# Kernel tuning notes

Hardware: AMD Instinct MI355X
Metric: run time of the kernel (lower is better)

## Reference

```python
import math
import jax, jax.numpy as jnp
import numpy as np

B, S, D = 4, 2048, 512
H = 8
HD = D // H  # 64


def setup_inputs() -> dict:
    key = jax.random.key(0)
    k1, k2, k3, k4, k5 = jax.random.split(key, 5)
    x = jax.random.normal(k1, (B, S, D), dtype=jnp.float32)
    # additive causal mask, broadcast over [H, B, S, S] in the original code
    neg_inf = jnp.float32(-1e9)
    mask = jnp.where(jnp.tril(jnp.ones((S, S), dtype=bool)), 0.0, neg_inf).astype(jnp.float32)
    Wqkv = jax.random.normal(k2, (D, 3 * D), dtype=jnp.float32) * (1.0 / math.sqrt(D))
    bqkv = jax.random.normal(k3, (3 * D,), dtype=jnp.float32) * 0.02
    Wo = jax.random.normal(k4, (D, D), dtype=jnp.float32) * (1.0 / math.sqrt(D))
    bo = jax.random.normal(k5, (D,), dtype=jnp.float32) * 0.02
    return {"x": x, "mask": mask, "Wqkv": Wqkv, "bqkv": bqkv, "Wo": Wo, "bo": bo}


def reference(x, mask, Wqkv, bqkv, Wo, bo):
    b, s, d = x.shape
    hd = d // H
    qkv = x @ Wqkv + bqkv                       # [b, s, 3d]
    # match torch: reshape to [b, s, H, 3*hd], move heads, chunk last dim
    qkv = qkv.reshape(b, s, H, 3 * hd).transpose(0, 2, 1, 3)  # [b, H, s, 3hd]
    q, k, v = jnp.split(qkv, 3, axis=-1)        # each [b, H, s, hd]
    scale = 1.0 / math.sqrt(hd)
    scores = jnp.einsum('bhqd,bhkd->bhqk', q, k) * scale
    scores = scores + mask                      # mask [s, s] broadcasts over [b, H, s, s]
    attn = jax.nn.softmax(scores, axis=-1)
    vals = jnp.einsum('bhqk,bhkd->bhqd', attn, v)
    vals = vals.transpose(0, 2, 1, 3).reshape(b, s, d)
    return vals @ Wo + bo
```

## Files before the change

### kernel.cpp

```cpp
#include <hip/hip_runtime.h>
#include <hip/hip_bf16.h>

#define S_ 2048
#define D_ 512
#define HD_ 64
#define HH_ 8
#define M_ 8192

typedef __attribute__((ext_vector_type(8))) short short8;
typedef __attribute__((ext_vector_type(4))) short short4v;
typedef __attribute__((ext_vector_type(4))) float f32x4;

__device__ __forceinline__ unsigned short f2bf(float f) {
  unsigned u = __builtin_bit_cast(unsigned, f);
  u += 0x7fffu + ((u >> 16) & 1u);
  return (unsigned short)(u >> 16);
}

__device__ __forceinline__ f32x4 mfma16(short8 a, short8 b, f32x4 c) {
  return __builtin_amdgcn_mfma_f32_16x16x32_bf16(a, b, c, 0, 0, 0);
}

#define GLOAD_LDS16(gp, lp)                                                        \
  __builtin_amdgcn_global_load_lds(                                                \
      (const __attribute__((address_space(1))) void*)(gp),                         \
      (__attribute__((address_space(3))) void*)(lp), 16, 0, 0)

__global__ __launch_bounds__(256) void k_cvt_bf16x8(const float* __restrict__ x,
                                                    short* __restrict__ o) {
  int idx = blockIdx.x * 256 + threadIdx.x;
  const float4* p = (const float4*)x;
  float4 a = p[idx * 2];
  float4 b = p[idx * 2 + 1];
  short8 v;
  v[0] = (short)f2bf(a.x); v[1] = (short)f2bf(a.y);
  v[2] = (short)f2bf(a.z); v[3] = (short)f2bf(a.w);
  v[4] = (short)f2bf(b.x); v[5] = (short)f2bf(b.y);
  v[6] = (short)f2bf(b.z); v[7] = (short)f2bf(b.w);
  int row = idx >> 6;
  int dst = row * 512 + ((idx >> 3) & 7) * 64 + (((idx & 7) ^ (row & 7)) << 3);
  *(short8*)&o[dst] = v;
}

__global__ __launch_bounds__(256) void k_cvt_transpose(const float* __restrict__ w,
                                                       short* __restrict__ wt,
                                                       int C) {
  __shared__ short T[32][33];
  const int tx = threadIdx.x & 31, ty = threadIdx.x >> 5;
  const int n0 = blockIdx.x * 32, k0 = blockIdx.y * 32;
#pragma unroll
  for (int i = 0; i < 4; i++) {
    int k = k0 + ty + 8 * i;
    T[ty + 8 * i][tx] = (short)f2bf(w[k * C + n0 + tx]);
  }
  __syncthreads();
#pragma unroll
  for (int i = 0; i < 4; i++) {
    int n = n0 + ty + 8 * i;
    int k = k0 + tx;
    int ksw = (k & ~63) | ((((k >> 3) & 7) ^ (n & 7)) << 3) | (k & 7);
    wt[n * 512 + ksw] = T[tx][ty + 8 * i];
  }
}

template <int MODE>
__global__ __launch_bounds__(256) void k_gemm(const short* __restrict__ A,
                                              const short* __restrict__ Bt,
                                              const float* __restrict__ bias,
                                              short* __restrict__ Qo,
                                              short* __restrict__ Ko,
                                              short* __restrict__ VTo,
                                              float* __restrict__ Fo) {
  __shared__ short As[2][8192];
  __shared__ short Bs[2][4096];
  const int tid = threadIdx.x;
  const int w = tid >> 6, l = tid & 63, g = l >> 4, c = l & 15;
  const int bm = blockIdx.x * 128, bn = blockIdx.y * 64;
  const int wm = (w >> 1) * 64, wn = (w & 1) * 32;
  f32x4 acc[4][2] = {};
  const short* Ap = A + (bm + (l >> 3)) * 512 + (l & 7) * 8;
  const short* Bp = Bt + (bn + (l >> 3)) * 512 + (l & 7) * 8;
  const int sa0 = w * 4;
  const int sb0 = w * 2;

#define GSTAGE(buf, k0)                                                       \
  {                                                                           \
    GLOAD_LDS16(Ap + (sa0 + 0) * 4096 + (k0), &As[buf][(sa0 + 0) * 512]);     \
    GLOAD_LDS16(Ap + (sa0 + 1) * 4096 + (k0), &As[buf][(sa0 + 1) * 512]);     \
    GLOAD_LDS16(Ap + (sa0 + 2) * 4096 + (k0), &As[buf][(sa0 + 2) * 512]);     \
    GLOAD_LDS16(Ap + (sa0 + 3) * 4096 + (k0), &As[buf][(sa0 + 3) * 512]);     \
    GLOAD_LDS16(Bp + (sb0 + 0) * 4096 + (k0), &Bs[buf][(sb0 + 0) * 512]);     \
    GLOAD_LDS16(Bp + (sb0 + 1) * 4096 + (k0), &Bs[buf][(sb0 + 1) * 512]);     \
  }

  GSTAGE(0, 0);
  __syncthreads();

  const int cs = c & 7;
  int cur = 0;
  for (int k0 = 0; k0 < 512; k0 += 64) {
    if (k0 + 64 < 512) GSTAGE(cur ^ 1, k0 + 64);

    short8 a0[4], a1[4], b0[2], b1[2];
#pragma unroll
    for (int mt = 0; mt < 4; mt++) {
      const short* r = &As[cur][(wm + mt * 16 + c) * 64];
      a0[mt] = *(const short8*)&r[(g ^ cs) << 3];
      a1[mt] = *(const short8*)&r[((g + 4) ^ cs) << 3];
    }
#pragma unroll
    for (int nt = 0; nt < 2; nt++) {
      const short* r = &Bs[cur][(wn + nt * 16 + c) * 64];
      b0[nt] = *(const short8*)&r[(g ^ cs) << 3];
      b1[nt] = *(const short8*)&r[((g + 4) ^ cs) << 3];
    }
#pragma unroll
    for (int mt = 0; mt < 4; mt++)
#pragma unroll
      for (int nt = 0; nt < 2; nt++) {
        acc[mt][nt] = mfma16(a0[mt], b0[nt], acc[mt][nt]);
        acc[mt][nt] = mfma16(a1[mt], b1[nt], acc[mt][nt]);
      }

    __syncthreads();
    cur ^= 1;
  }
#undef GSTAGE

  if (MODE == 0) {
    const float QS = 0.125f * 1.4426950408889634f;
#pragma unroll
    for (int nt = 0; nt < 2; nt++) {
      int n = bn + wn + nt * 16 + c;
      float bv = bias[n];
      int h = n / 192;
      int t = n - h * 192;
      int type = t >> 6;
      int hd = t & 63;
      float sc = (type == 0) ? QS : 1.0f;
#pragma unroll
      for (int mt = 0; mt < 4; mt++) {
        int m0 = bm + wm + mt * 16 + 4 * g;
        int b = m0 >> 11, ss = m0 & 2047;
        int bh = b * 8 + h;
        if (type == 2) {
          int sw = (ss & ~63) | (((((ss >> 3) & 7) ^ (hd & 7)) << 3)) | (ss & 7);
          short4v pk;
#pragma unroll
          for (int r = 0; r < 4; r++) pk[r] = (short)f2bf(acc[mt][nt][r] + bv);
          *(short4v*)&VTo[(bh * 64 + hd) * 2048 + sw] = pk;
        } else if (type == 1) {
#pragma unroll
          for (int r = 0; r < 4; r++) {
            int s = ss + r;
            int hds = ((((hd >> 3) ^ (s & 7)) << 3)) | (hd & 7);
            Ko[(bh * 2048 + s) * 64 + hds] = (short)f2bf(acc[mt][nt][r] + bv);
          }
        } else {
#pragma unroll
          for (int r = 0; r < 4; r++)
            Qo[(bh * 2048 + ss + r) * 64 + hd] = (short)f2bf((acc[mt][nt][r] + bv) * sc);
        }
      }
    }
  } else {
#pragma unroll
    for (int nt = 0; nt < 2; nt++) {
      int n = bn + wn + nt * 16 + c;
      float bv = bias[n];
#pragma unroll
      for (int mt = 0; mt < 4; mt++) {
        int m0 = bm + wm + mt * 16 + 4 * g;
#pragma unroll
        for (int r = 0; r < 4; r++) Fo[(m0 + r) * 512 + n] = acc[mt][nt][r] + bv;
      }
    }
  }
}

__global__ __launch_bounds__(256, 4) void k_attn(const short* __restrict__ Q,
                                                 const short* __restrict__ K,
                                                 const short* __restrict__ VT,
                                                 short* __restrict__ ctx) {
  __shared__ short Ks[2][4096];
  __shared__ short Vs[2][4096];
  __shared__ short P[4][1024];
  const int tid = threadIdx.x;
  const int w = tid >> 6, l = tid & 63, g = l >> 4, c = l & 15;

  const int x = blockIdx.x;
  const int bh = x & 31;
  const int jc = 31 - (x >> 5);
  const int qbase = jc * 64 + w * 16;
  const int ntiles = jc + 1;

  const short* Qb = Q + bh * S_ * HD_;
  const short* Kb = K + bh * S_ * HD_;
  const short* Vb = VT + bh * HD_ * S_;

  const int i0 = tid, i1 = tid + 256;
  const int kr0 = i0 >> 3, kc0 = (i0 & 7) * 8;
  const int kr1 = i1 >> 3, kc1 = (i1 & 7) * 8;
  short* KL0 = &Ks[0][w * 512];
  short* KL1 = &Ks[0][2048 + w * 512];
  short* VL0 = &Vs[0][w * 512];
  short* VL1 = &Vs[0][2048 + w * 512];

#define STAGE(buf, kv0)                                                     \
  {                                                                         \
    GLOAD_LDS16(Kb + ((kv0) + kr0) * 64 + kc0, KL0 + (buf)*4096);           \
    GLOAD_LDS16(Kb + ((kv0) + kr1) * 64 + kc1, KL1 + (buf)*4096);           \
    GLOAD_LDS16(Vb + kr0 * 2048 + (kv0) + kc0, VL0 + (buf)*4096);           \
    GLOAD_LDS16(Vb + kr1 * 2048 + (kv0) + kc1, VL1 + (buf)*4096);           \
  }

  short* Pw = &P[w][0];
  const int bb = bh >> 3, hh = bh & 7;
  const f32x4 CINIT = {-16.f, -16.f, -16.f, -16.f};

  short8 qf0 = *(const short8*)&Qb[(qbase + c) * 64 + 8 * g];
  short8 qf1 = *(const short8*)&Qb[(qbase + c) * 64 + 8 * g + 32];

  f32x4 o[4];
  float psum[4];
#pragma unroll
  for (int nt = 0; nt < 4; nt++) o[nt] = f32x4{0.f, 0.f, 0.f, 0.f};
#pragma unroll
  for (int r = 0; r < 4; r++) psum[r] = 0.f;

  STAGE(0, 0);
  __syncthreads();

  int cur = 0;
  for (int it = 0; it < ntiles; ++it) {
    const int kv0 = it * 64;
    if (it + 1 < ntiles) STAGE(cur ^ 1, kv0 + 64);

    const short* Kt = &Ks[cur][0];
    const short* Vt = &Vs[cur][0];

    f32x4 sa[4];
#pragma unroll
    for (int nt = 0; nt < 4; nt++) {
      short8 kf0 = *(const short8*)&Kt[((nt * 16 + c) << 6) + ((g ^ (c & 7)) << 3)];
      short8 kf1 = *(const short8*)&Kt[((nt * 16 + c) << 6) + (((g + 4) ^ (c & 7)) << 3)];
      sa[nt] = mfma16(qf0, kf0, CINIT);
      sa[nt] = mfma16(qf1, kf1, sa[nt]);
    }

    if (kv0 + 64 > qbase) {
#pragma unroll
      for (int nt = 0; nt < 4; nt++) {
        int kv = kv0 + nt * 16 + c;
#pragma unroll
        for (int r = 0; r < 4; r++) {
          int qrow = qbase + 4 * g + r;
          if (kv > qrow) sa[nt][r] = -1e30f;
        }
      }
    }

#pragma unroll
    for (int nt = 0; nt < 4; nt++)
#pragma unroll
      for (int r = 0; r < 4; r++) {
        float pv = __builtin_amdgcn_exp2f(sa[nt][r]);
        psum[r] += pv;
        int row = 4 * g + r;
        int col = nt * 16 + c;
        int off = (row << 6) + ((((col >> 3) ^ (row & 7)) << 3)) + (col & 7);
        Pw[off] = (short)f2bf(pv);
      }

#pragma unroll
    for (int kvb = 0; kvb < 2; kvb++) {
      short8 pa = *(const short8*)&Pw[(c << 6) + (((kvb * 4 + g) ^ (c & 7)) << 3)];
#pragma unroll
      for (int nt = 0; nt < 4; nt++) {
        short8 vb = *(const short8*)&Vt[((nt * 16 + c) << 6) +
                                        (((kvb * 4 + g) ^ (c & 7)) << 3)];
        o[nt] = mfma16(pa, vb, o[nt]);
      }
    }

    __syncthreads();
    cur ^= 1;
  }

#pragma unroll
  for (int off = 1; off < 16; off <<= 1)
#pragma unroll
    for (int r = 0; r < 4; r++) psum[r] += __shfl_xor(psum[r], off, 64);

  float inv[4];
#pragma unroll
  for (int r = 0; r < 4; r++) inv[r] = 1.0f / psum[r];
#pragma unroll
  for (int nt = 0; nt < 4; nt++)
#pragma unroll
    for (int r = 0; r < 4; r++) {
      int srow = qbase + 4 * g + r;
      int colsw = hh * 64 + (((nt * 2 + (c >> 3)) ^ (srow & 7)) << 3) + (c & 7);
      ctx[(bb * S_ + srow) * 512 + colsw] = (short)f2bf(o[nt][r] * inv[r]);
    }
#undef STAGE
}


extern "C" void kernel_launch(void* const* d_in, const int* in_sizes, int n_in,
                              void* d_out, int out_size, void* d_ws, size_t ws_size,
                              hipStream_t stream) {
  const float* x = (const float*)d_in[0];
  const float* Wqkv = (const float*)d_in[2];
  const float* bqkv = (const float*)d_in[3];
  const float* Wo = (const float*)d_in[4];
  const float* bo = (const float*)d_in[5];
  float* out = (float*)d_out;

  char* ws = (char*)d_ws;
  short* xb    = (short*)(ws + 0);
  short* wqkvt = (short*)(ws + 8388608);
  short* wot   = (short*)(ws + 9961472);
  short* Qw    = (short*)(ws + 10485760);
  short* Kw    = (short*)(ws + 18874368);
  short* VTw   = (short*)(ws + 27262976);
  short* ctx   = (short*)(ws + 35651584);

  k_cvt_bf16x8<<<2048, 256, 0, stream>>>(x, xb);
  {
    dim3 gt(48, 16);
    k_cvt_transpose<<<gt, 256, 0, stream>>>(Wqkv, wqkvt, 1536);
    dim3 gt2(16, 16);
    k_cvt_transpose<<<gt2, 256, 0, stream>>>(Wo, wot, 512);
  }

  dim3 g1(64, 24);
  k_gemm<0><<<g1, 256, 0, stream>>>(xb, wqkvt, bqkv, Qw, Kw, VTw, nullptr);

  k_attn<<<1024, 256, 0, stream>>>(Qw, Kw, VTw, ctx);

  dim3 g3(64, 8);
  k_gemm<1><<<g3, 256, 0, stream>>>(ctx, wot, bo, nullptr, nullptr, nullptr, out);
}
```

Measured before the change: 85.23 us.

## Split attention KV tile across two wave groups with 512-thread blocks

Doubles the attention block to 8 waves: each group of four waves takes half of every 64-key tile (32 keys), computes partial scores, P and PV accumulations, and the two partial outputs and row sums are combined through LDS at the end. Staging loads are spread over twice as many threads. The aim is more waves in flight per query tile to hide latency and shorten the serial KV loop per wave, at the cost of an extra reduction through shared memory and a final barrier. Launch bounds are raised to 512 threads with a higher minimum block count, which may constrain registers.

Result: slower. 95.01 us (+11.5%).

```diff
diff --git a/kernel.cpp b/kernel.cpp
--- a/kernel.cpp
+++ b/kernel.cpp
@@ -178,40 +178,32 @@
   }
 }
 
-__global__ __launch_bounds__(256, 4) void k_attn(const short* __restrict__ Q,
+__global__ __launch_bounds__(512, 8) void k_attn(const short* __restrict__ Q,
                                                  const short* __restrict__ K,
                                                  const short* __restrict__ VT,
                                                  short* __restrict__ ctx) {
-  __shared__ short Ks[2][4096];
-  __shared__ short Vs[2][4096];
-  __shared__ short P[4][1024];
+  __shared__ short KVs[2][8192];
+  __shared__ short P[8][512];
   const int tid = threadIdx.x;
   const int w = tid >> 6, l = tid & 63, g = l >> 4, c = l & 15;
+  const int rg = w & 3, pp = w >> 2;
 
   const int x = blockIdx.x;
   const int bh = x & 31;
-  const int jc = 31 - (x >> 5);
-  const int qbase = jc * 64 + w * 16;
-  const int ntiles = jc + 1;
+  const int j = 31 - (x >> 5);
+  const int qbase = j * 64 + rg * 16;
+  const int nss = j + 1;
 
   const short* Qb = Q + bh * S_ * HD_;
   const short* Kb = K + bh * S_ * HD_;
   const short* Vb = VT + bh * HD_ * S_;
 
-  const int i0 = tid, i1 = tid + 256;
-  const int kr0 = i0 >> 3, kc0 = (i0 & 7) * 8;
-  const int kr1 = i1 >> 3, kc1 = (i1 & 7) * 8;
-  short* KL0 = &Ks[0][w * 512];
-  short* KL1 = &Ks[0][2048 + w * 512];
-  short* VL0 = &Vs[0][w * 512];
-  short* VL1 = &Vs[0][2048 + w * 512];
-
-#define STAGE(buf, kv0)                                                     \
-  {                                                                         \
-    GLOAD_LDS16(Kb + ((kv0) + kr0) * 64 + kc0, KL0 + (buf)*4096);           \
-    GLOAD_LDS16(Kb + ((kv0) + kr1) * 64 + kc1, KL1 + (buf)*4096);           \
-    GLOAD_LDS16(Vb + kr0 * 2048 + (kv0) + kc0, VL0 + (buf)*4096);           \
-    GLOAD_LDS16(Vb + kr1 * 2048 + (kv0) + kc1, VL1 + (buf)*4096);           \
+  const int kr = tid >> 3, kc8 = (tid & 7) * 8;
+
+#define STAGE(buf, kv0)                                                      \
+  {                                                                          \
+    GLOAD_LDS16(Kb + ((kv0) + kr) * 64 + kc8, &KVs[buf][w * 512]);           \
+    GLOAD_LDS16(Vb + kr * 2048 + (kv0) + kc8, &KVs[buf][4096 + w * 512]);    \
   }
 
   short* Pw = &P[w][0];
@@ -232,25 +224,26 @@
   __syncthreads();
 
   int cur = 0;
-  for (int it = 0; it < ntiles; ++it) {
-    const int kv0 = it * 64;
-    if (it + 1 < ntiles) STAGE(cur ^ 1, kv0 + 64);
-
-    const short* Kt = &Ks[cur][0];
-    const short* Vt = &Vs[cur][0];
-
-    f32x4 sa[4];
-#pragma unroll
-    for (int nt = 0; nt < 4; nt++) {
-      short8 kf0 = *(const short8*)&Kt[((nt * 16 + c) << 6) + ((g ^ (c & 7)) << 3)];
-      short8 kf1 = *(const short8*)&Kt[((nt * 16 + c) << 6) + (((g + 4) ^ (c & 7)) << 3)];
+  for (int t = 0; t < nss; ++t) {
+    if (t + 1 < nss) STAGE(cur ^ 1, (t + 1) * 64);
+
+    const short* Kt = &KVs[cur][pp * 2048];
+    const short* Vt = &KVs[cur][4096];
+    const int kv0 = t * 64 + pp * 32;
+
+    f32x4 sa[2];
+#pragma unroll
+    for (int nt = 0; nt < 2; nt++) {
+      const short* r = &Kt[(nt * 16 + c) * 64];
+      short8 kf0 = *(const short8*)&r[(g ^ (c & 7)) << 3];
+      short8 kf1 = *(const short8*)&r[((g + 4) ^ (c & 7)) << 3];
       sa[nt] = mfma16(qf0, kf0, CINIT);
       sa[nt] = mfma16(qf1, kf1, sa[nt]);
     }
 
-    if (kv0 + 64 > qbase) {
-#pragma unroll
-      for (int nt = 0; nt < 4; nt++) {
+    if (kv0 + 32 > qbase) {
+#pragma unroll
+      for (int nt = 0; nt < 2; nt++) {
         int kv = kv0 + nt * 16 + c;
 #pragma unroll
         for (int r = 0; r < 4; r++) {
@@ -261,26 +254,23 @@
     }
 
 #pragma unroll
-    for (int nt = 0; nt < 4; nt++)
+    for (int nt = 0; nt < 2; nt++)
 #pragma unroll
       for (int r = 0; r < 4; r++) {
         float pv = __builtin_amdgcn_exp2f(sa[nt][r]);
         psum[r] += pv;
         int row = 4 * g + r;
         int col = nt * 16 + c;
-        int off = (row << 6) + ((((col >> 3) ^ (row & 7)) << 3)) + (col & 7);
+        int off = (row << 5) + ((((col >> 3) ^ (row & 3)) << 3)) + (col & 7);
         Pw[off] = (short)f2bf(pv);
       }
 
-#pragma unroll
-    for (int kvb = 0; kvb < 2; kvb++) {
-      short8 pa = *(const short8*)&Pw[(c << 6) + (((kvb * 4 + g) ^ (c & 7)) << 3)];
-#pragma unroll
-      for (int nt = 0; nt < 4; nt++) {
-        short8 vb = *(const short8*)&Vt[((nt * 16 + c) << 6) +
-                                        (((kvb * 4 + g) ^ (c & 7)) << 3)];
-        o[nt] = mfma16(pa, vb, o[nt]);
-      }
+    short8 pa = *(const short8*)&Pw[(c << 5) + ((g ^ (c & 3)) << 3)];
+#pragma unroll
+    for (int nt = 0; nt < 4; nt++) {
+      short8 vb = *(const short8*)&Vt[((nt * 16 + c) << 6) +
+                                      (((4 * pp + g) ^ (c & 7)) << 3)];
+      o[nt] = mfma16(pa, vb, o[nt]);
     }
 
     __syncthreads();
@@ -292,17 +282,35 @@
 #pragma unroll
     for (int r = 0; r < 4; r++) psum[r] += __shfl_xor(psum[r], off, 64);
 
-  float inv[4];
-#pragma unroll
-  for (int r = 0; r < 4; r++) inv[r] = 1.0f / psum[r];
-#pragma unroll
-  for (int nt = 0; nt < 4; nt++)
-#pragma unroll
-    for (int r = 0; r < 4; r++) {
-      int srow = qbase + 4 * g + r;
-      int colsw = hh * 64 + (((nt * 2 + (c >> 3)) ^ (srow & 7)) << 3) + (c & 7);
-      ctx[(bb * S_ + srow) * 512 + colsw] = (short)f2bf(o[nt][r] * inv[r]);
-    }
+  float* scr = (float*)&KVs[0][0];
+  float* pscr = (float*)&P[0][0];
+  if (pp == 1) {
+#pragma unroll
+    for (int nt = 0; nt < 4; nt++)
+#pragma unroll
+      for (int r = 0; r < 4; r++)
+        scr[rg * 1088 + (4 * g + r) * 68 + nt * 16 + c] = o[nt][r];
+    if (c == 0) {
+#pragma unroll
+      for (int r = 0; r < 4; r++) pscr[rg * 16 + 4 * g + r] = psum[r];
+    }
+  }
+  __syncthreads();
+  if (pp == 0) {
+    float inv[4];
+#pragma unroll
+    for (int r = 0; r < 4; r++)
+      inv[r] = 1.0f / (psum[r] + pscr[rg * 16 + 4 * g + r]);
+#pragma unroll
+    for (int nt = 0; nt < 4; nt++)
+#pragma unroll
+      for (int r = 0; r < 4; r++) {
+        float ov = o[nt][r] + scr[rg * 1088 + (4 * g + r) * 68 + nt * 16 + c];
+        int srow = qbase + 4 * g + r;
+        int colsw = hh * 64 + (((nt * 2 + (c >> 3)) ^ (srow & 7)) << 3) + (c & 7);
+        ctx[(bb * S_ + srow) * 512 + colsw] = (short)f2bf(ov * inv[r]);
+      }
+  }
 #undef STAGE
 }
 
@@ -337,7 +345,7 @@
   dim3 g1(64, 24);
   k_gemm<0><<<g1, 256, 0, stream>>>(xb, wqkvt, bqkv, Qw, Kw, VTw, nullptr);
 
-  k_attn<<<1024, 256, 0, stream>>>(Qw, Kw, VTw, ctx);
+  k_attn<<<1024, 512, 0, stream>>>(Qw, Kw, VTw, ctx);
 
   dim3 g3(64, 8);
   k_gemm<1><<<g3, 256, 0, stream>>>(ctx, wot, bo, nullptr, nullptr, nullptr, out);
```
